# Optimization experiments

Measured on AMD Instinct MI355X. Metric: run time of the kernel, lower is better.

The kernel has to match this reference:

```python
import jax, jax.numpy as jnp
import numpy as np

NUM_BINS = 4
NUM_CELLS = NUM_BINS ** 3


def _generate_grids(num_bins):
    # cell-center coordinates in the unit cube, matching generate_grids()
    c = (jnp.arange(num_bins, dtype=jnp.float32) + 1.0) / num_bins - 0.5 / num_bins
    gx, gy, gz = jnp.meshgrid(c, c, c, indexing='ij')
    return jnp.stack([gx.ravel(), gy.ravel(), gz.ravel()], axis=1)  # [C, 3]


def setup_inputs() -> dict:
    key = jax.random.key(0)
    x = jax.random.normal(key, (64, 65536, 6), dtype=jnp.float32)
    return {"input": x}


def reference(input):
    B, P, _ = input.shape
    pos = input[..., 0:3]
    ori = input[..., 3:6]

    # symmetric bounding cube: bbox_max over points and xyz dims
    bbox_max = jnp.max(jnp.abs(pos), axis=(1, 2), keepdims=True)          # [B,1,1]
    thickness = jnp.clip(2.0 * bbox_max, 1e-5, None)
    pos_in_cube = (pos + bbox_max) / thickness                            # [B,P,3] in [0,1]

    ci = jnp.clip((pos_in_cube * NUM_BINS).astype(jnp.int32), 0, NUM_BINS - 1)
    cell_idx = (ci[..., 0] * NUM_BINS + ci[..., 1]) * NUM_BINS + ci[..., 2]  # [B,P]

    seg = lambda vals, idx: jax.ops.segment_sum(vals, idx, num_segments=NUM_CELLS)

    # per-cell point counts
    freq = jax.vmap(seg)(jnp.ones((B, P), jnp.float32), cell_idx)[..., None]  # [B,C,1]
    freq_c = jnp.clip(freq, 1.0, None)
    uprefix = 1.0 / jnp.sqrt(freq_c)
    f_freq = 0.001 * freq * uprefix                                       # [B,C,1]

    # mean offset from cell centers
    grids = _generate_grids(NUM_BINS)                                     # [C,3]
    offsets = pos_in_cube - grids[cell_idx]                               # [B,P,3]
    f_mean = jax.vmap(seg)(offsets, cell_idx) * uprefix                   # [B,C,3]

    # upper-triangular orientation covariance: xx,xy,xz,yy,yz,zz
    ox, oy, oz = ori[..., 0], ori[..., 1], ori[..., 2]
    cov = jnp.stack([ox * ox, ox * oy, ox * oz, oy * oy, oy * oz, oz * oz], axis=-1)  # [B,P,6]
    f_normcov = jax.vmap(seg)(cov, cell_idx) / freq_c                     # [B,C,6]

    f_all = jnp.concatenate([f_freq, f_mean, f_normcov], axis=2).reshape(B, -1)  # [B, C*10]
    norm = jnp.linalg.norm(f_all, axis=1, keepdims=True)
    return f_all / jnp.clip(norm, 1e-12, None)
```

## Files before the change

### kernel.cpp

```cpp
#include <hip/hip_runtime.h>


#define BATCH 64
#define NPTS 65536
#define FEAT 640
#define COPIES 16
#define CSTRIDE 17
#define S_OFF 262144.0f
#define S_COV 4096.0f

__device__ __forceinline__ void bin_point(int* h, int k,
                                          float px, float py, float pz,
                                          float ox, float oy, float oz,
                                          float bmax, float inv_thick) {
    float sx = (px + bmax) * inv_thick;
    float sy = (py + bmax) * inv_thick;
    float sz = (pz + bmax) * inv_thick;
    int cx = (int)(sx * 4.0f); cx = cx < 0 ? 0 : (cx > 3 ? 3 : cx);
    int cy = (int)(sy * 4.0f); cy = cy < 0 ? 0 : (cy > 3 ? 3 : cy);
    int cz = (int)(sz * 4.0f); cz = cz < 0 ? 0 : (cz > 3 ? 3 : cz);
    int cell = (cx * 4 + cy) * 4 + cz;
    float offx = sx - (cx * 0.25f + 0.125f);
    float offy = sy - (cy * 0.25f + 0.125f);
    float offz = sz - (cz * 0.25f + 0.125f);
    int a = cell * (10 * CSTRIDE) + k;
    atomicAdd(&h[a + 0 * CSTRIDE], 1);
    atomicAdd(&h[a + 1 * CSTRIDE], __float2int_rn(offx * S_OFF));
    atomicAdd(&h[a + 2 * CSTRIDE], __float2int_rn(offy * S_OFF));
    atomicAdd(&h[a + 3 * CSTRIDE], __float2int_rn(offz * S_OFF));
    atomicAdd(&h[a + 4 * CSTRIDE], __float2int_rn(ox * ox * S_COV));
    atomicAdd(&h[a + 5 * CSTRIDE], __float2int_rn(ox * oy * S_COV));
    atomicAdd(&h[a + 6 * CSTRIDE], __float2int_rn(ox * oz * S_COV));
    atomicAdd(&h[a + 7 * CSTRIDE], __float2int_rn(oy * oy * S_COV));
    atomicAdd(&h[a + 8 * CSTRIDE], __float2int_rn(oy * oz * S_COV));
    atomicAdd(&h[a + 9 * CSTRIDE], __float2int_rn(oz * oz * S_COV));
}

__global__ __launch_bounds__(256) void k_bbox(const float* __restrict__ x,
                                              unsigned int* __restrict__ part,
                                              unsigned long long* __restrict__ acc) {
    int b = blockIdx.y;
    int fb = b * 16 + blockIdx.x;
    if (threadIdx.x < 40) acc[fb * 40 + threadIdx.x] = 0ULL;

    const float4* base = (const float4*)(x + (size_t)b * NPTS * 6);
    int tid = blockIdx.x * 256 + threadIdx.x;
    float m = 0.0f;
    #pragma unroll
    for (int it = 0; it < 8; ++it) {
        int i = tid + it * 4096;
        float4 f0 = base[3 * i + 0];
        float4 f1 = base[3 * i + 1];
        float4 f2 = base[3 * i + 2];
        m = fmaxf(m, fabsf(f0.x)); m = fmaxf(m, fabsf(f0.y)); m = fmaxf(m, fabsf(f0.z));
        m = fmaxf(m, fabsf(f1.z)); m = fmaxf(m, fabsf(f1.w)); m = fmaxf(m, fabsf(f2.x));
    }
    for (int off = 32; off > 0; off >>= 1) m = fmaxf(m, __shfl_down(m, off, 64));
    __shared__ float s[4];
    if ((threadIdx.x & 63) == 0) s[threadIdx.x >> 6] = m;
    __syncthreads();
    if (threadIdx.x == 0) {
        m = fmaxf(fmaxf(s[0], s[1]), fmaxf(s[2], s[3]));
        part[fb] = __float_as_uint(m);
    }
}

__global__ __launch_bounds__(256) void k_bin(const float* __restrict__ x,
                                             const unsigned int* __restrict__ part,
                                             unsigned long long* __restrict__ acc) {
    __shared__ int h[FEAT * CSTRIDE];
    for (int i = threadIdx.x; i < FEAT * CSTRIDE; i += 256) h[i] = 0;
    int b = blockIdx.y;
    unsigned int um = 0u;
    #pragma unroll
    for (int p = 0; p < 16; ++p) um = um > part[b * 16 + p] ? um : part[b * 16 + p];
    float bmax = __uint_as_float(um);
    float thick = fmaxf(2.0f * bmax, 1e-5f);
    float inv_thick = 1.0f / thick;
    __syncthreads();

    const float4* base = (const float4*)(x + (size_t)b * NPTS * 6);
    int tid = blockIdx.x * 256 + threadIdx.x;
    int k = threadIdx.x & (COPIES - 1);
    #pragma unroll
    for (int it = 0; it < 8; ++it) {
        int i = tid + it * 4096;
        float4 f0 = base[3 * i + 0];
        float4 f1 = base[3 * i + 1];
        float4 f2 = base[3 * i + 2];
        bin_point(h, k, f0.x, f0.y, f0.z, f0.w, f1.x, f1.y, bmax, inv_thick);
        bin_point(h, k, f1.z, f1.w, f2.x, f2.y, f2.z, f2.w, bmax, inv_thick);
    }
    __syncthreads();
    for (int v = threadIdx.x; v < FEAT; v += 256) {
        long long sum = 0;
        #pragma unroll
        for (int c = 0; c < COPIES; ++c) sum += (long long)h[v * CSTRIDE + c];
        atomicAdd(&acc[b * FEAT + v], (unsigned long long)sum);
    }
}

__global__ __launch_bounds__(640) void k_final(const unsigned long long* __restrict__ acc,
                                               float* __restrict__ out) {
    int b = blockIdx.x;
    int t = threadIdx.x;
    int cell = t / 10, j = t - cell * 10;
    long long ni = (long long)acc[b * FEAT + cell * 10];
    long long vi = (long long)acc[b * FEAT + t];
    float n = (float)ni;
    float fc = fmaxf(n, 1.0f);
    float up = 1.0f / sqrtf(fc);
    float val;
    if (j == 0)      val = 0.001f * n * up;
    else if (j < 4)  val = ((float)vi * (1.0f / S_OFF)) * up;
    else             val = ((float)vi * (1.0f / S_COV)) / fc;

    __shared__ float red[12];
    float s = val * val;
    for (int off = 32; off > 0; off >>= 1) s += __shfl_down(s, off, 64);
    if ((t & 63) == 0) red[t >> 6] = s;
    __syncthreads();
    if (t == 0) {
        float tot = 0.0f;
        #pragma unroll
        for (int w = 0; w < 10; ++w) tot += red[w];
        red[10] = fmaxf(sqrtf(tot), 1e-12f);
    }
    __syncthreads();
    out[b * FEAT + t] = val / red[10];
}

extern "C" void kernel_launch(void* const* d_in, const int* in_sizes, int n_in,
                              void* d_out, int out_size, void* d_ws, size_t ws_size,
                              hipStream_t stream) {
    const float* x = (const float*)d_in[0];
    float* out = (float*)d_out;
    unsigned int* part = (unsigned int*)d_ws;
    unsigned long long* acc = (unsigned long long*)((char*)d_ws + 4096);

    dim3 grid(16, BATCH);
    k_bbox<<<grid, 256, 0, stream>>>(x, part, acc);
    k_bin<<<grid, 256, 0, stream>>>(x, part, acc);
    k_final<<<BATCH, 640, 0, stream>>>(acc, out);
}
```

Measured before the change: 164.5 us.

## Fuse final normalization into binning kernel via last-block counter; XOR-swizzle histogram copies

Removes the separate k_final launch. Each batch keeps a done counter, and the last k_bin block to finish for that batch reads the accumulated sums, computes the norm and writes the output. Separately, the shared histogram stride drops from 17 to 16, and the per-thread copy index is XOR-swizzled by cell so bank conflicts stay low while shared memory shrinks. This saves one kernel launch and its gap, at the cost of an agent-scope atomic and a serialized tail in the last block per batch.

```diff
diff --git a/kernel.cpp b/kernel.cpp
--- a/kernel.cpp
+++ b/kernel.cpp
@@ -5,7 +5,7 @@
 #define NPTS 65536
 #define FEAT 640
 #define COPIES 16
-#define CSTRIDE 17
+#define CSTRIDE 16
 #define S_OFF 262144.0f
 #define S_COV 4096.0f
 
@@ -23,7 +23,8 @@
     float offx = sx - (cx * 0.25f + 0.125f);
     float offy = sy - (cy * 0.25f + 0.125f);
     float offz = sz - (cz * 0.25f + 0.125f);
-    int a = cell * (10 * CSTRIDE) + k;
+    int kk = k ^ (cell & 15);
+    int a = cell * (10 * CSTRIDE) + kk;
     atomicAdd(&h[a + 0 * CSTRIDE], 1);
     atomicAdd(&h[a + 1 * CSTRIDE], __float2int_rn(offx * S_OFF));
     atomicAdd(&h[a + 2 * CSTRIDE], __float2int_rn(offy * S_OFF));
@@ -38,10 +39,12 @@
 
 __global__ __launch_bounds__(256) void k_bbox(const float* __restrict__ x,
                                               unsigned int* __restrict__ part,
+                                              int* __restrict__ done,
                                               unsigned long long* __restrict__ acc) {
     int b = blockIdx.y;
     int fb = b * 16 + blockIdx.x;
     if (threadIdx.x < 40) acc[fb * 40 + threadIdx.x] = 0ULL;
+    if (blockIdx.x == 0 && threadIdx.x == 64) done[b] = 0;
 
     const float4* base = (const float4*)(x + (size_t)b * NPTS * 6);
     int tid = blockIdx.x * 256 + threadIdx.x;
@@ -67,9 +70,13 @@
 
 __global__ __launch_bounds__(256) void k_bin(const float* __restrict__ x,
                                              const unsigned int* __restrict__ part,
-                                             unsigned long long* __restrict__ acc) {
+                                             int* __restrict__ done,
+                                             unsigned long long* __restrict__ acc,
+                                             float* __restrict__ out) {
     __shared__ int h[FEAT * CSTRIDE];
-    for (int i = threadIdx.x; i < FEAT * CSTRIDE; i += 256) h[i] = 0;
+    float* hf = (float*)h;
+    int t = threadIdx.x;
+    for (int i = t; i < FEAT * CSTRIDE; i += 256) h[i] = 0;
     int b = blockIdx.y;
     unsigned int um = 0u;
     #pragma unroll
@@ -80,8 +87,8 @@
     __syncthreads();
 
     const float4* base = (const float4*)(x + (size_t)b * NPTS * 6);
-    int tid = blockIdx.x * 256 + threadIdx.x;
-    int k = threadIdx.x & (COPIES - 1);
+    int tid = blockIdx.x * 256 + t;
+    int k = t & (COPIES - 1);
     #pragma unroll
     for (int it = 0; it < 8; ++it) {
         int i = tid + it * 4096;
@@ -92,42 +99,61 @@
         bin_point(h, k, f1.z, f1.w, f2.x, f2.y, f2.z, f2.w, bmax, inv_thick);
     }
     __syncthreads();
-    for (int v = threadIdx.x; v < FEAT; v += 256) {
+    for (int v = t; v < FEAT; v += 256) {
         long long sum = 0;
         #pragma unroll
         for (int c = 0; c < COPIES; ++c) sum += (long long)h[v * CSTRIDE + c];
         atomicAdd(&acc[b * FEAT + v], (unsigned long long)sum);
     }
-}
+    __syncthreads();
 
-__global__ __launch_bounds__(640) void k_final(const unsigned long long* __restrict__ acc,
-                                               float* __restrict__ out) {
-    int b = blockIdx.x;
-    int t = threadIdx.x;
-    int cell = t / 10, j = t - cell * 10;
-    long long ni = (long long)acc[b * FEAT + cell * 10];
-    long long vi = (long long)acc[b * FEAT + t];
-    float n = (float)ni;
-    float fc = fmaxf(n, 1.0f);
-    float up = 1.0f / sqrtf(fc);
-    float val;
-    if (j == 0)      val = 0.001f * n * up;
-    else if (j < 4)  val = ((float)vi * (1.0f / S_OFF)) * up;
-    else             val = ((float)vi * (1.0f / S_COV)) / fc;
+    if (t == 0) {
+        int old = __hip_atomic_fetch_add(&done[b], 1, __ATOMIC_ACQ_REL,
+                                         __HIP_MEMORY_SCOPE_AGENT);
+        h[0] = (old == 15) ? 1 : 0;
+    }
+    __syncthreads();
+    if (h[0] == 0) return;
+    __syncthreads();
 
-    __shared__ float red[12];
-    float s = val * val;
-    for (int off = 32; off > 0; off >>= 1) s += __shfl_down(s, off, 64);
-    if ((t & 63) == 0) red[t >> 6] = s;
+    float sq = 0.0f;
+    float vals[3];
+    #pragma unroll
+    for (int r = 0; r < 3; ++r) {
+        int v = t + r * 256;
+        float val = 0.0f;
+        if (v < FEAT) {
+            int cell = v / 10, j = v - cell * 10;
+            unsigned long long nu = __hip_atomic_load(&acc[b * FEAT + cell * 10],
+                                                      __ATOMIC_RELAXED,
+                                                      __HIP_MEMORY_SCOPE_AGENT);
+            unsigned long long vu = __hip_atomic_load(&acc[b * FEAT + v],
+                                                      __ATOMIC_RELAXED,
+                                                      __HIP_MEMORY_SCOPE_AGENT);
+            float n = (float)(long long)nu;
+            float fc = fmaxf(n, 1.0f);
+            float up = 1.0f / sqrtf(fc);
+            if (j == 0)      val = 0.001f * n * up;
+            else if (j < 4)  val = ((float)(long long)vu * (1.0f / S_OFF)) * up;
+            else             val = ((float)(long long)vu * (1.0f / S_COV)) / fc;
+            sq += val * val;
+        }
+        vals[r] = val;
+    }
+    for (int off = 32; off > 0; off >>= 1) sq += __shfl_down(sq, off, 64);
+    if ((t & 63) == 0) hf[1024 + (t >> 6)] = sq;
     __syncthreads();
     if (t == 0) {
-        float tot = 0.0f;
-        #pragma unroll
-        for (int w = 0; w < 10; ++w) tot += red[w];
-        red[10] = fmaxf(sqrtf(tot), 1e-12f);
+        float tot = hf[1024] + hf[1025] + hf[1026] + hf[1027];
+        hf[1028] = fmaxf(sqrtf(tot), 1e-12f);
     }
     __syncthreads();
-    out[b * FEAT + t] = val / red[10];
+    float norm = hf[1028];
+    #pragma unroll
+    for (int r = 0; r < 3; ++r) {
+        int v = t + r * 256;
+        if (v < FEAT) out[b * FEAT + v] = vals[r] / norm;
+    }
 }
 
 extern "C" void kernel_launch(void* const* d_in, const int* in_sizes, int n_in,
@@ -136,10 +162,10 @@
     const float* x = (const float*)d_in[0];
     float* out = (float*)d_out;
     unsigned int* part = (unsigned int*)d_ws;
-    unsigned long long* acc = (unsigned long long*)((char*)d_ws + 4096);
+    int* done = (int*)((char*)d_ws + 4096);
+    unsigned long long* acc = (unsigned long long*)((char*)d_ws + 8192);
 
     dim3 grid(16, BATCH);
-    k_bbox<<<grid, 256, 0, stream>>>(x, part, acc);
-    k_bin<<<grid, 256, 0, stream>>>(x, part, acc);
-    k_final<<<BATCH, 640, 0, stream>>>(acc, out);
+    k_bbox<<<grid, 256, 0, stream>>>(x, part, done, acc);
+    k_bin<<<grid, 256, 0, stream>>>(x, part, done, acc, out);
 }
```

Measured after the change: 188.6 us. +14.6%, slower.
